# Optimization experiments

Hardware: AMD Instinct MI355X
Metric: run time of the kernel (lower is better)

## Reference

```python
import jax, jax.numpy as jnp
import numpy as np

E = 1024
H = 16
D = E // H
RANK = 4
NLANG = 8
SCALING = D ** -0.5


def _lowrank(r, s):
    # r: [rank, out], s: [rank, in] -> sum of outer products [out, in]
    return jnp.einsum('ro,ri->oi', r, s)


def setup_inputs() -> dict:
    key = jax.random.key(0)
    ks = jax.random.split(key, 20)
    std = np.sqrt(2.0 / (E + E)).astype(np.float32)
    std_lr = np.sqrt(0.02).astype(np.float32)
    inp = {
        'query': jax.random.normal(ks[0], (1024, 8, E), jnp.float32),
        'key': jax.random.normal(ks[1], (1024, 8, E), jnp.float32),
        'in_proj_weight_q': jax.random.normal(ks[2], (E, E), jnp.float32) * std,
        'in_proj_weight_kv': jax.random.normal(ks[3], (2 * E, E), jnp.float32) * std,
        'out_proj_weight': jax.random.normal(ks[4], (E, E), jnp.float32) * std,
        'r_q': jax.random.normal(ks[5], (NLANG, RANK, E), jnp.float32) * std_lr,
        's_q': jax.random.normal(ks[6], (NLANG, RANK, E), jnp.float32) * std_lr,
        'r_kv': jax.random.normal(ks[7], (NLANG, RANK, 2 * E), jnp.float32) * std_lr,
        's_kv': jax.random.normal(ks[8], (NLANG, RANK, E), jnp.float32) * std_lr,
        'r_o': jax.random.normal(ks[9], (NLANG, RANK, E), jnp.float32) * std_lr,
        's_o': jax.random.normal(ks[10], (NLANG, RANK, E), jnp.float32) * std_lr,
        # multiplicative factors: random +/-1 as in bernoulli init
        'rm_q': jnp.sign(jax.random.normal(ks[11], (NLANG, RANK, E), jnp.float32)),
        'sm_q': jnp.sign(jax.random.normal(ks[12], (NLANG, RANK, E), jnp.float32)),
        'rm_kv': jnp.sign(jax.random.normal(ks[13], (NLANG, RANK, 2 * E), jnp.float32)),
        'sm_kv': jnp.sign(jax.random.normal(ks[14], (NLANG, RANK, E), jnp.float32)),
        'rm_o': jnp.sign(jax.random.normal(ks[15], (NLANG, RANK, E), jnp.float32)),
        'sm_o': jnp.sign(jax.random.normal(ks[16], (NLANG, RANK, E), jnp.float32)),
        'src_indices': jax.random.randint(ks[17], (1,), 0, NLANG, jnp.int64 if jax.config.jax_enable_x64 else jnp.int32),
        'tgt_indices': jax.random.randint(ks[18], (1,), 0, NLANG, jnp.int64 if jax.config.jax_enable_x64 else jnp.int32),
    }
    return inp


def reference(query, key, in_proj_weight_q, in_proj_weight_kv, out_proj_weight,
              r_q, s_q, r_kv, s_kv, r_o, s_o,
              rm_q, sm_q, rm_kv, sm_kv, rm_o, sm_o,
              src_indices, tgt_indices):
    it = tgt_indices[0]
    isrc = src_indices[0]

    # multiplicative low-rank modulation then additive low-rank update
    Wq = in_proj_weight_q * _lowrank(rm_q[it], sm_q[isrc]) + _lowrank(r_q[it], s_q[isrc])
    Wkv = in_proj_weight_kv * _lowrank(rm_kv[it], sm_kv[isrc]) + _lowrank(r_kv[it], s_kv[isrc])
    Wo = out_proj_weight * _lowrank(rm_o[it], sm_o[isrc]) + _lowrank(r_o[it], s_o[isrc])

    lq, b, _ = query.shape
    lk = key.shape[0]

    # projections: F.linear(x, W) = x @ W.T
    q = jnp.einsum('lbe,fe->lbf', query, Wq) * SCALING          # [lq, b, E]
    kv = jnp.einsum('lbe,fe->lbf', key, Wkv)                    # [lk, b, 2E]
    k, v = kv[..., :E], kv[..., E:]

    # split heads: [len, b, E] -> [b*H, len, D]
    def to_heads(x, L):
        return x.reshape(L, b, H, D).transpose(1, 2, 0, 3).reshape(b * H, L, D)

    qh = to_heads(q, lq)
    kh = to_heads(k, lk)
    vh = to_heads(v, lk)

    scores = jnp.einsum('nqd,nkd->nqk', qh, kh)                 # [b*H, lq, lk]
    probs = jax.nn.softmax(scores, axis=-1)
    ctx = jnp.einsum('nqk,nkd->nqd', probs, vh)                 # [b*H, lq, D]

    # merge heads back to [lq, b, E]
    ctx = ctx.reshape(b, H, lq, D).transpose(2, 0, 1, 3).reshape(lq, b, E)
    out = jnp.einsum('lbe,fe->lbf', ctx, Wo)
    return out, probs
```

## Files before the change

### kernel.cpp

```cpp
#include <hip/hip_runtime.h>
#include <hip/hip_bf16.h>


typedef float  fx4 __attribute__((ext_vector_type(4)));
typedef short  sx8 __attribute__((ext_vector_type(8)));
typedef _Float16 hx8 __attribute__((ext_vector_type(8)));

__device__ __forceinline__ unsigned short f2h(float f) {
  return __builtin_bit_cast(unsigned short, (_Float16)f);
}
__device__ __forceinline__ float h2f(unsigned short h) {
  return (float)__builtin_bit_cast(_Float16, h);
}
__device__ __forceinline__ unsigned pk2h(float a, float b) {
  return __builtin_bit_cast(unsigned, __builtin_amdgcn_cvt_pkrtz(a, b));
}

__device__ __forceinline__ void gload_lds16(const void* g, void* l) {
  __builtin_amdgcn_global_load_lds((const __attribute__((address_space(1))) void*)g,
                                   (__attribute__((address_space(3))) void*)l, 16, 0, 0);
}

__device__ __forceinline__ fx4 mfma_h(sx8 a, sx8 b, fx4 c) {
  return __builtin_amdgcn_mfma_f32_16x16x32_f16(__builtin_bit_cast(hx8, a),
                                                __builtin_bit_cast(hx8, b), c, 0, 0, 0);
}

__device__ __forceinline__ void wait_vm_bar() {
  __builtin_amdgcn_sched_barrier(0);
  asm volatile("s_waitcnt vmcnt(0)" ::: "memory");
  __builtin_amdgcn_s_barrier();
  __builtin_amdgcn_sched_barrier(0);
}
__device__ __forceinline__ void wait_vm4_bar() {
  __builtin_amdgcn_sched_barrier(0);
  asm volatile("s_waitcnt vmcnt(4)" ::: "memory");
  __builtin_amdgcn_s_barrier();
  __builtin_amdgcn_sched_barrier(0);
}
__device__ __forceinline__ void bar_only() {
  __builtin_amdgcn_sched_barrier(0);
  __builtin_amdgcn_s_barrier();
  __builtin_amdgcn_sched_barrier(0);
}
__device__ __forceinline__ void bar_lgkm() {
  __builtin_amdgcn_sched_barrier(0);
  asm volatile("s_waitcnt lgkmcnt(0)" ::: "memory");
  __builtin_amdgcn_s_barrier();
  __builtin_amdgcn_sched_barrier(0);
}

__global__ void k_prep(
    const float* wq, const float* wkv, const float* wo,
    const float* r_q, const float* s_q, const float* r_kv, const float* s_kv,
    const float* r_o, const float* s_o,
    const float* rm_q, const float* sm_q, const float* rm_kv, const float* sm_kv,
    const float* rm_o, const float* sm_o,
    const int* src_i, const int* tgt_i,
    unsigned short* Wq16, unsigned short* Wkv16, unsigned short* Wo16,
    const float* query, const float* key,
    unsigned short* qh, unsigned short* kh)
{
  const int gid = blockIdx.x * 256 + threadIdx.x;
  if (gid >= 4194304) {
    const int cid = gid - 4194304;
    const bool isq = cid < 1048576;
    const size_t off = (size_t)(isq ? cid : cid - 1048576) * 8;
    const float* s = (isq ? query : key) + off;
    unsigned short* d = (isq ? qh : kh) + off;
    fx4 a = *(const fx4*)s, bv = *(const fx4*)(s + 4);
    sx8 h;
    #pragma unroll
    for (int j = 0; j < 4; ++j) { h[j] = (short)f2h(a[j]); h[4 + j] = (short)f2h(bv[j]); }
    *(sx8*)d = h;
    return;
  }
  const int it = tgt_i[0], is = src_i[0];
  const int mat = gid >> 20;
  const int idx = gid & 1048575;
  const int o = idx >> 10, i = idx & 1023;
  float lrm = 0.f, lr = 0.f;
  if (mat == 0) {
    #pragma unroll
    for (int r = 0; r < 4; ++r) {
      lrm += rm_q[(it * 4 + r) * 1024 + o] * sm_q[(is * 4 + r) * 1024 + i];
      lr  += r_q [(it * 4 + r) * 1024 + o] * s_q [(is * 4 + r) * 1024 + i];
    }
    Wq16[idx] = f2h((wq[idx] * lrm + lr) * 0.125f);
  } else if (mat == 1) {
    #pragma unroll
    for (int r = 0; r < 4; ++r) {
      lrm += rm_kv[(it * 4 + r) * 2048 + o] * sm_kv[(is * 4 + r) * 1024 + i];
      lr  += r_kv [(it * 4 + r) * 2048 + o] * s_kv [(is * 4 + r) * 1024 + i];
    }
    Wkv16[idx] = f2h(wkv[idx] * lrm + lr);
  } else if (mat == 2) {
    #pragma unroll
    for (int r = 0; r < 4; ++r) {
      lrm += rm_kv[(it * 4 + r) * 2048 + 1024 + o] * sm_kv[(is * 4 + r) * 1024 + i];
      lr  += r_kv [(it * 4 + r) * 2048 + 1024 + o] * s_kv [(is * 4 + r) * 1024 + i];
    }
    Wkv16[1048576 + idx] = f2h(wkv[1048576 + idx] * lrm + lr);
  } else {
    #pragma unroll
    for (int r = 0; r < 4; ++r) {
      lrm += rm_o[(it * 4 + r) * 1024 + o] * sm_o[(is * 4 + r) * 1024 + i];
      lr  += r_o [(it * 4 + r) * 1024 + o] * s_o [(is * 4 + r) * 1024 + i];
    }
    Wo16[idx] = f2h(wo[idx] * lrm + lr);
  }
}

__global__ __launch_bounds__(256, 2) void k_gemm_kvq(
    const unsigned short* qh, const unsigned short* kh,
    const unsigned short* Wq16, const unsigned short* Wkv16,
    unsigned short* k16, unsigned short* v16, unsigned short* q16)
{
  __shared__ unsigned short lds[2][2][4096];
  const int tid = threadIdx.x;
  const int l = tid & 63, wid = tid >> 6;
  const int wr = wid >> 1, wc = wid & 1;
  const int bid = blockIdx.x;
  const int logical = (bid & 7) * 192 + (bid >> 3);
  const int by = logical / 24, bx = logical % 24;
  const bool isKV = bx < 16;
  const unsigned short* A = isKV ? kh : qh;
  const unsigned short* B = isKV ? Wkv16 : Wq16;
  const int mBase = by * 128;
  const int nBase = (isKV ? bx : (bx - 16)) * 128;
  const int brow = tid >> 2, bc8 = (tid & 3) * 8;

  fx4 acc[4][4] = {};

  auto stage = [&](int buf, int kt) {
    const int kB = kt * 32;
    gload_lds16(B + (size_t)(nBase + brow) * 1024 + kB + bc8,      &lds[buf][1][tid * 8]);
    gload_lds16(B + (size_t)(nBase + 64 + brow) * 1024 + kB + bc8, &lds[buf][1][2048 + tid * 8]);
    gload_lds16(A + (size_t)(mBase + brow) * 1024 + kB + bc8,      &lds[buf][0][tid * 8]);
    gload_lds16(A + (size_t)(mBase + 64 + brow) * 1024 + kB + bc8, &lds[buf][0][2048 + tid * 8]);
  };

  auto compute = [&](int buf) {
    sx8 af[4], bfv[4];
    #pragma unroll
    for (int x = 0; x < 4; ++x) {
      af[x]  = *(const sx8*)&lds[buf][0][(wr * 64 + x * 16 + (l & 15)) * 32 + (l >> 4) * 8];
      bfv[x] = *(const sx8*)&lds[buf][1][(wc * 64 + x * 16 + (l & 15)) * 32 + (l >> 4) * 8];
    }
    #pragma unroll
    for (int mi = 0; mi < 4; ++mi)
      #pragma unroll
      for (int ni = 0; ni < 4; ++ni)
        acc[mi][ni] = mfma_h(af[mi], bfv[ni], acc[mi][ni]);
  };

  stage(0, 0);
  for (int kt = 0; kt < 32; ++kt) {
    const int buf = kt & 1;
    if (kt + 1 < 32) {
      stage(buf ^ 1, kt + 1);
      wait_vm4_bar();
    } else {
      wait_vm_bar();
    }
    compute(buf);
    bar_only();
  }

  #pragma unroll
  for (int mi = 0; mi < 4; ++mi)
    #pragma unroll
    for (int ni = 0; ni < 4; ++ni)
      #pragma unroll
      for (int i = 0; i < 4; ++i) {
        const size_t row = (size_t)(mBase + wr * 64 + mi * 16 + (l >> 4) * 4 + i);
        const int col = nBase + wc * 64 + ni * 16 + (l & 15);
        const unsigned short hv = f2h(acc[mi][ni][i]);
        if (isKV) {
          if (col < 1024) k16[row * 1024 + col] = hv;
          else            v16[row * 1024 + (col - 1024)] = hv;
        } else {
          q16[row * 1024 + col] = hv;
        }
      }
}

__global__ __launch_bounds__(256, 2) void k_gemm_out(
    const unsigned short* A, const unsigned short* B, float* Cf)
{
  __shared__ unsigned short lds[2][2][4096];
  const int tid = threadIdx.x;
  const int l = tid & 63, wid = tid >> 6;
  const int wr = wid >> 1, wc = wid & 1;
  const int bid = blockIdx.x;
  const int logical = (bid & 7) * 64 + (bid >> 3);
  const int mBase = (logical >> 3) * 128, nBase = (logical & 7) * 128;
  const int brow = tid >> 2, bc8 = (tid & 3) * 8;

  fx4 acc[4][4] = {};

  auto stage = [&](int buf, int kt) {
    const int kB = kt * 32;
    gload_lds16(B + (size_t)(nBase + brow) * 1024 + kB + bc8,      &lds[buf][1][tid * 8]);
    gload_lds16(B + (size_t)(nBase + 64 + brow) * 1024 + kB + bc8, &lds[buf][1][2048 + tid * 8]);
    gload_lds16(A + (size_t)(mBase + brow) * 1024 + kB + bc8,      &lds[buf][0][tid * 8]);
    gload_lds16(A + (size_t)(mBase + 64 + brow) * 1024 + kB + bc8, &lds[buf][0][2048 + tid * 8]);
  };

  auto compute = [&](int buf) {
    sx8 af[4], bfv[4];
    #pragma unroll
    for (int x = 0; x < 4; ++x) {
      af[x]  = *(const sx8*)&lds[buf][0][(wr * 64 + x * 16 + (l & 15)) * 32 + (l >> 4) * 8];
      bfv[x] = *(const sx8*)&lds[buf][1][(wc * 64 + x * 16 + (l & 15)) * 32 + (l >> 4) * 8];
    }
    #pragma unroll
    for (int mi = 0; mi < 4; ++mi)
      #pragma unroll
      for (int ni = 0; ni < 4; ++ni)
        acc[mi][ni] = mfma_h(af[mi], bfv[ni], acc[mi][ni]);
  };

  stage(0, 0);
  for (int kt = 0; kt < 32; ++kt) {
    const int buf = kt & 1;
    if (kt + 1 < 32) {
      stage(buf ^ 1, kt + 1);
      wait_vm4_bar();
    } else {
      wait_vm_bar();
    }
    compute(buf);
    bar_only();
  }

  #pragma unroll
  for (int mi = 0; mi < 4; ++mi)
    #pragma unroll
    for (int ni = 0; ni < 4; ++ni)
      #pragma unroll
      for (int i = 0; i < 4; ++i) {
        const size_t row = (size_t)(mBase + wr * 64 + mi * 16 + (l >> 4) * 4 + i);
        const int col = nBase + wc * 64 + ni * 16 + (l & 15);
        __builtin_nontemporal_store(acc[mi][ni][i], &Cf[row * 1024 + col]);
      }
}

__global__ __launch_bounds__(256) void k_vt(const unsigned short* v16, unsigned short* vT)
{
  __shared__ unsigned short t[64 * 72];
  const int tid = threadIdx.x;
  const int head = blockIdx.x >> 4, kb = blockIdx.x & 15;
  const int b = head >> 4, hh = head & 15;
  const int kl = tid >> 2, part = tid & 3;
  #pragma unroll
  for (int u = 0; u < 2; ++u) {
    sx8 v = *(const sx8*)&v16[(size_t)((kb * 64 + kl) * 8 + b) * 1024 + hh * 64 + part * 16 + u * 8];
    *(sx8*)&t[kl * 72 + part * 16 + u * 8] = v;
  }
  __syncthreads();
  const int dr = tid >> 2;
  unsigned short out[16];
  #pragma unroll
  for (int j = 0; j < 16; ++j) out[j] = t[(part * 16 + j) * 72 + dr];
  unsigned short* dst = vT + (size_t)((b * 16 + hh) * 64 + dr) * 1024 + kb * 64 + part * 16;
  *(sx8*)dst       = *(sx8*)&out[0];
  *(sx8*)(dst + 8) = *(sx8*)&out[8];
}

__global__ __launch_bounds__(512, 4) void k_attn(
    const unsigned short* q16, const unsigned short* k16, const unsigned short* vT,
    float* probsF, unsigned short* ctx)
{
  __shared__ __align__(16) unsigned short Pl[32768];
  __shared__ float redm[128], reds[128];

  const int tid = threadIdx.x, l = tid & 63, wid = tid >> 6;
  const int qg = wid >> 2, q4 = wid & 3;
  const int r = l & 15, g = l >> 4;
  const int bid = blockIdx.x;
  const int logical = (bid & 7) * 512 + (bid >> 3);
  const int head = logical >> 5, qb = logical & 31;
  const int b = head >> 4, hh = head & 15;

  auto stage_k = [&](int c) {
    #pragma unroll
    for (int rr = 0; rr < 8; ++rr) {
      const int e = rr * 512 + tid;
      const int lk = e >> 3, ch = e & 7;
      gload_lds16(k16 + (size_t)((c * 512 + lk) * 8 + b) * 1024 + hh * 64 + ((ch ^ (lk & 7)) * 8),
                  &Pl[e * 8]);
    }
  };

  sx8 qf0, qf1;
  {
    const int qrow = qb * 32 + qg * 16 + r;
    const size_t qoff = (size_t)(qrow * 8 + b) * 1024 + hh * 64 + g * 8;
    qf0 = *(const sx8*)&q16[qoff];
    qf1 = *(const sx8*)&q16[qoff + 32];
  }

  fx4 acc[16];
  #pragma unroll
  for (int s = 0; s < 16; ++s) acc[s] = fx4{0.f, 0.f, 0.f, 0.f};

  stage_k(0);
  wait_vm_bar();
  #pragma unroll
  for (int t = 0; t < 8; ++t) {
    const int lk = q4 * 128 + t * 16 + r;
    sx8 kb0 = *(const sx8*)&Pl[lk * 64 + ((g ^ (l & 7))) * 8];
    sx8 kb1 = *(const sx8*)&Pl[lk * 64 + (((4 + g) ^ (l & 7))) * 8];
    acc[t] = mfma_h(kb0, qf0, acc[t]);
    acc[t] = mfma_h(kb1, qf1, acc[t]);
  }
  bar_lgkm();
  stage_k(1);
  wait_vm_bar();
  #pragma unroll
  for (int t = 0; t < 8; ++t) {
    const int lk = q4 * 128 + t * 16 + r;
    sx8 kb0 = *(const sx8*)&Pl[lk * 64 + ((g ^ (l & 7))) * 8];
    sx8 kb1 = *(const sx8*)&Pl[lk * 64 + (((4 + g) ^ (l & 7))) * 8];
    acc[8 + t] = mfma_h(kb0, qf0, acc[8 + t]);
    acc[8 + t] = mfma_h(kb1, qf1, acc[8 + t]);
  }

  const int q = qg * 16 + r;
  float m = -3e38f;
  #pragma unroll
  for (int s = 0; s < 16; ++s)
    #pragma unroll
    for (int i = 0; i < 4; ++i) m = fmaxf(m, acc[s][i]);
  m = fmaxf(m, __shfl_xor(m, 16));
  m = fmaxf(m, __shfl_xor(m, 32));
  if (g == 0) redm[q * 4 + q4] = m;
  bar_lgkm();
  const float mf = fmaxf(fmaxf(redm[q * 4], redm[q * 4 + 1]),
                         fmaxf(redm[q * 4 + 2], redm[q * 4 + 3]));
  float ssum = 0.f;
  #pragma unroll
  for (int s = 0; s < 16; ++s)
    #pragma unroll
    for (int i = 0; i < 4; ++i) {
      const float e = __expf(acc[s][i] - mf);
      acc[s][i] = e;
      ssum += e;
    }
  ssum += __shfl_xor(ssum, 16);
  ssum += __shfl_xor(ssum, 32);
  if (g == 0) reds[q * 4 + q4] = ssum;
  bar_lgkm();
  const float inv = 1.0f / (reds[q * 4] + reds[q * 4 + 1] +
                            reds[q * 4 + 2] + reds[q * 4 + 3]);

  #pragma unroll
  for (int idx = 0; idx < 16; ++idx) {
    const int c = idx >> 3, t = idx & 7;
    const int k0 = c * 512 + q4 * 128 + t * 16 + g * 4;
    uint2 w;
    w.x = pk2h(acc[idx][0] * inv, acc[idx][1] * inv);
    w.y = pk2h(acc[idx][2] * inv, acc[idx][3] * inv);
    *(uint2*)&Pl[q * 1024 + (((k0 >> 3) ^ (q & 7)) << 3) + (k0 & 7)] = w;
  }
  bar_lgkm();

  if (wid < 4) {
    fx4 cacc0 = {}, cacc1 = {};
    const unsigned short* vrow = vT + (size_t)((b * 16 + hh) * 64 + wid * 16 + r) * 1024;
    #pragma unroll
    for (int cc = 0; cc < 32; ++cc) {
      const int k0 = cc * 32 + g * 8;
      sx8 vb  = *(const sx8*)&vrow[k0];
      sx8 pa0 = *(const sx8*)&Pl[(0 * 16 + r) * 1024 + (((k0 >> 3) ^ (r & 7)) << 3)];
      sx8 pa1 = *(const sx8*)&Pl[(16 + r) * 1024 + (((k0 >> 3) ^ ((16 + r) & 7)) << 3)];
      cacc0 = mfma_h(pa0, vb, cacc0);
      cacc1 = mfma_h(pa1, vb, cacc1);
    }
    const int d = wid * 16 + r;
    #pragma unroll
    for (int i = 0; i < 4; ++i) {
      const int q0 = qb * 32 + g * 4 + i;
      const int q1 = qb * 32 + 16 + g * 4 + i;
      ctx[(size_t)(q0 * 8 + b) * 1024 + hh * 64 + d] = f2h(cacc0[i]);
      ctx[(size_t)(q1 * 8 + b) * 1024 + hh * 64 + d] = f2h(cacc1[i]);
    }
  } else {
    const size_t pbase = (size_t)head * 1048576;
    const int rbase = (wid - 4) * 8;
    #pragma unroll
    for (int i = 0; i < 32; ++i) {
      const int row = rbase + (i >> 2);
      const int col = (i & 3) * 256 + l * 4;
      const int c16 = ((col >> 3) ^ (row & 7));
      const unsigned* raw = (const unsigned*)&Pl[row * 1024 + c16 * 8 + (col & 7)];
      const unsigned r0 = raw[0], r1 = raw[1];
      fx4 o;
      o[0] = h2f((unsigned short)(r0 & 0xffffu)); o[1] = h2f((unsigned short)(r0 >> 16));
      o[2] = h2f((unsigned short)(r1 & 0xffffu)); o[3] = h2f((unsigned short)(r1 >> 16));
      __builtin_nontemporal_store(o, (fx4*)&probsF[pbase + (size_t)(qb * 32 + row) * 1024 + col]);
    }
  }
}

extern "C" void kernel_launch(void* const* d_in, const int* in_sizes, int n_in,
                              void* d_out, int out_size, void* d_ws, size_t ws_size,
                              hipStream_t stream)
{
  const float* query = (const float*)d_in[0];
  const float* key   = (const float*)d_in[1];
  const float* wq    = (const float*)d_in[2];
  const float* wkv   = (const float*)d_in[3];
  const float* wo    = (const float*)d_in[4];
  const float* r_q   = (const float*)d_in[5];
  const float* s_q   = (const float*)d_in[6];
  const float* r_kv  = (const float*)d_in[7];
  const float* s_kv  = (const float*)d_in[8];
  const float* r_o   = (const float*)d_in[9];
  const float* s_o   = (const float*)d_in[10];
  const float* rm_q  = (const float*)d_in[11];
  const float* sm_q  = (const float*)d_in[12];
  const float* rm_kv = (const float*)d_in[13];
  const float* sm_kv = (const float*)d_in[14];
  const float* rm_o  = (const float*)d_in[15];
  const float* sm_o  = (const float*)d_in[16];
  const int* src_i   = (const int*)d_in[17];
  const int* tgt_i   = (const int*)d_in[18];

  unsigned short* ws16 = (unsigned short*)d_ws;
  const size_t M1 = 1048576, M8 = 8388608;
  unsigned short* Wq16  = ws16;
  unsigned short* Wkv16 = ws16 + M1;
  unsigned short* Wo16  = ws16 + 3 * M1;
  unsigned short* qh    = ws16 + 4 * M1;
  unsigned short* kh    = ws16 + 12 * M1;
  unsigned short* k16   = ws16 + 20 * M1;
  unsigned short* v16   = ws16 + 28 * M1;
  unsigned short* vT  = kh;
  unsigned short* ctx = qh;

  float* outF   = (float*)d_out;
  float* probsF = outF + M8;
  unsigned short* q16 = (unsigned short*)outF;

  k_prep<<<dim3(24576), dim3(256), 0, stream>>>(
      wq, wkv, wo, r_q, s_q, r_kv, s_kv, r_o, s_o,
      rm_q, sm_q, rm_kv, sm_kv, rm_o, sm_o, src_i, tgt_i,
      Wq16, Wkv16, Wo16, query, key, qh, kh);

  k_gemm_kvq<<<dim3(1536), dim3(256), 0, stream>>>(
      qh, kh, Wq16, Wkv16, k16, v16, q16);

  k_vt<<<dim3(2048), dim3(256), 0, stream>>>(v16, vT);

  k_attn<<<dim3(4096), dim3(512), 0, stream>>>(q16, k16, vT, probsF, ctx);

  k_gemm_out<<<dim3(512), dim3(256), 0, stream>>>(ctx, Wo16, outF);
}
```

Before: 272.7 us.

## Triple-buffer GEMM LDS pipeline and use nontemporal loads for streamed inputs

Both projection GEMMs move from double to triple buffering of LDS tiles, prefetching two k-steps ahead with a vmcnt(8) wait, and the launch bound rises to 3 blocks per CU. The aim is to hide more global-load latency behind MFMA work. Streaming reads in the prep and V-transpose kernels become nontemporal loads so they pollute the cache less. The extra buffer raises LDS use to 48KB per block and may constrain registers under the higher occupancy target.

```diff
diff --git a/kernel.cpp b/kernel.cpp
--- a/kernel.cpp
+++ b/kernel.cpp
@@ -29,6 +29,12 @@
 __device__ __forceinline__ void wait_vm_bar() {
   __builtin_amdgcn_sched_barrier(0);
   asm volatile("s_waitcnt vmcnt(0)" ::: "memory");
+  __builtin_amdgcn_s_barrier();
+  __builtin_amdgcn_sched_barrier(0);
+}
+__device__ __forceinline__ void wait_vm8_bar() {
+  __builtin_amdgcn_sched_barrier(0);
+  asm volatile("s_waitcnt vmcnt(8)" ::: "memory");
   __builtin_amdgcn_s_barrier();
   __builtin_amdgcn_sched_barrier(0);
 }
@@ -68,7 +74,8 @@
     const size_t off = (size_t)(isq ? cid : cid - 1048576) * 8;
     const float* s = (isq ? query : key) + off;
     unsigned short* d = (isq ? qh : kh) + off;
-    fx4 a = *(const fx4*)s, bv = *(const fx4*)(s + 4);
+    fx4 a = __builtin_nontemporal_load((const fx4*)s);
+    fx4 bv = __builtin_nontemporal_load((const fx4*)(s + 4));
     sx8 h;
     #pragma unroll
     for (int j = 0; j < 4; ++j) { h[j] = (short)f2h(a[j]); h[4 + j] = (short)f2h(bv[j]); }
@@ -86,37 +93,37 @@
       lrm += rm_q[(it * 4 + r) * 1024 + o] * sm_q[(is * 4 + r) * 1024 + i];
       lr  += r_q [(it * 4 + r) * 1024 + o] * s_q [(is * 4 + r) * 1024 + i];
     }
-    Wq16[idx] = f2h((wq[idx] * lrm + lr) * 0.125f);
+    Wq16[idx] = f2h((__builtin_nontemporal_load(&wq[idx]) * lrm + lr) * 0.125f);
   } else if (mat == 1) {
     #pragma unroll
     for (int r = 0; r < 4; ++r) {
       lrm += rm_kv[(it * 4 + r) * 2048 + o] * sm_kv[(is * 4 + r) * 1024 + i];
       lr  += r_kv [(it * 4 + r) * 2048 + o] * s_kv [(is * 4 + r) * 1024 + i];
     }
-    Wkv16[idx] = f2h(wkv[idx] * lrm + lr);
+    Wkv16[idx] = f2h(__builtin_nontemporal_load(&wkv[idx]) * lrm + lr);
   } else if (mat == 2) {
     #pragma unroll
     for (int r = 0; r < 4; ++r) {
       lrm += rm_kv[(it * 4 + r) * 2048 + 1024 + o] * sm_kv[(is * 4 + r) * 1024 + i];
       lr  += r_kv [(it * 4 + r) * 2048 + 1024 + o] * s_kv [(is * 4 + r) * 1024 + i];
     }
-    Wkv16[1048576 + idx] = f2h(wkv[1048576 + idx] * lrm + lr);
+    Wkv16[1048576 + idx] = f2h(__builtin_nontemporal_load(&wkv[1048576 + idx]) * lrm + lr);
   } else {
     #pragma unroll
     for (int r = 0; r < 4; ++r) {
       lrm += rm_o[(it * 4 + r) * 1024 + o] * sm_o[(is * 4 + r) * 1024 + i];
       lr  += r_o [(it * 4 + r) * 1024 + o] * s_o [(is * 4 + r) * 1024 + i];
     }
-    Wo16[idx] = f2h(wo[idx] * lrm + lr);
-  }
-}
-
-__global__ __launch_bounds__(256, 2) void k_gemm_kvq(
+    Wo16[idx] = f2h(__builtin_nontemporal_load(&wo[idx]) * lrm + lr);
+  }
+}
+
+__global__ __launch_bounds__(256, 3) void k_gemm_kvq(
     const unsigned short* qh, const unsigned short* kh,
     const unsigned short* Wq16, const unsigned short* Wkv16,
     unsigned short* k16, unsigned short* v16, unsigned short* q16)
 {
-  __shared__ unsigned short lds[2][2][4096];
+  __shared__ unsigned short lds[3][2][4096];
   const int tid = threadIdx.x;
   const int l = tid & 63, wid = tid >> 6;
   const int wr = wid >> 1, wc = wid & 1;
@@ -155,10 +162,13 @@
   };
 
   stage(0, 0);
+  stage(1, 1);
   for (int kt = 0; kt < 32; ++kt) {
-    const int buf = kt & 1;
-    if (kt + 1 < 32) {
-      stage(buf ^ 1, kt + 1);
+    const int buf = kt % 3;
+    if (kt + 2 < 32) {
+      stage((kt + 2) % 3, kt + 2);
+      wait_vm8_bar();
+    } else if (kt == 30) {
       wait_vm4_bar();
     } else {
       wait_vm_bar();
@@ -185,10 +195,10 @@
       }
 }
 
-__global__ __launch_bounds__(256, 2) void k_gemm_out(
+__global__ __launch_bounds__(256, 3) void k_gemm_out(
     const unsigned short* A, const unsigned short* B, float* Cf)
 {
-  __shared__ unsigned short lds[2][2][4096];
+  __shared__ unsigned short lds[3][2][4096];
   const int tid = threadIdx.x;
   const int l = tid & 63, wid = tid >> 6;
   const int wr = wid >> 1, wc = wid & 1;
@@ -222,10 +232,13 @@
   };
 
   stage(0, 0);
+  stage(1, 1);
   for (int kt = 0; kt < 32; ++kt) {
-    const int buf = kt & 1;
-    if (kt + 1 < 32) {
-      stage(buf ^ 1, kt + 1);
+    const int buf = kt % 3;
+    if (kt + 2 < 32) {
+      stage((kt + 2) % 3, kt + 2);
+      wait_vm8_bar();
+    } else if (kt == 30) {
       wait_vm4_bar();
     } else {
       wait_vm_bar();
@@ -255,7 +268,8 @@
   const int kl = tid >> 2, part = tid & 3;
   #pragma unroll
   for (int u = 0; u < 2; ++u) {
-    sx8 v = *(const sx8*)&v16[(size_t)((kb * 64 + kl) * 8 + b) * 1024 + hh * 64 + part * 16 + u * 8];
+    sx8 v = __builtin_nontemporal_load(
+        (const sx8*)&v16[(size_t)((kb * 64 + kl) * 8 + b) * 1024 + hh * 64 + part * 16 + u * 8]);
     *(sx8*)&t[kl * 72 + part * 16 + u * 8] = v;
   }
   __syncthreads();
```

New measurement: 279.4 us. 2.5% more time.

## Fuse V transpose into KV projection GEMM epilogue and use nontemporal loads in prep

Applied to the files above, without the earlier changes.

The V half of the KV projection GEMM now writes its tile transposed through shared memory straight into the per-head vT layout, so the separate k_vt kernel is gone. This drops one launch and a full write-plus-read round trip of the V tensor through global memory. The prep kernel also switches its streaming fp32 loads to nontemporal loads. In exchange, the GEMM needs extra LDS for the transpose buffer, which may lower occupancy, and its V-tile epilogue issues 16 strided 2-byte LDS reads per output chunk.

```diff
diff --git a/kernel.cpp b/kernel.cpp
--- a/kernel.cpp
+++ b/kernel.cpp
@@ -68,7 +68,8 @@
     const size_t off = (size_t)(isq ? cid : cid - 1048576) * 8;
     const float* s = (isq ? query : key) + off;
     unsigned short* d = (isq ? qh : kh) + off;
-    fx4 a = *(const fx4*)s, bv = *(const fx4*)(s + 4);
+    fx4 a = __builtin_nontemporal_load((const fx4*)s);
+    fx4 bv = __builtin_nontemporal_load((const fx4*)(s + 4));
     sx8 h;
     #pragma unroll
     for (int j = 0; j < 4; ++j) { h[j] = (short)f2h(a[j]); h[4 + j] = (short)f2h(bv[j]); }
@@ -86,37 +87,38 @@
       lrm += rm_q[(it * 4 + r) * 1024 + o] * sm_q[(is * 4 + r) * 1024 + i];
       lr  += r_q [(it * 4 + r) * 1024 + o] * s_q [(is * 4 + r) * 1024 + i];
     }
-    Wq16[idx] = f2h((wq[idx] * lrm + lr) * 0.125f);
+    Wq16[idx] = f2h((__builtin_nontemporal_load(&wq[idx]) * lrm + lr) * 0.125f);
   } else if (mat == 1) {
     #pragma unroll
     for (int r = 0; r < 4; ++r) {
       lrm += rm_kv[(it * 4 + r) * 2048 + o] * sm_kv[(is * 4 + r) * 1024 + i];
       lr  += r_kv [(it * 4 + r) * 2048 + o] * s_kv [(is * 4 + r) * 1024 + i];
     }
-    Wkv16[idx] = f2h(wkv[idx] * lrm + lr);
+    Wkv16[idx] = f2h(__builtin_nontemporal_load(&wkv[idx]) * lrm + lr);
   } else if (mat == 2) {
     #pragma unroll
     for (int r = 0; r < 4; ++r) {
       lrm += rm_kv[(it * 4 + r) * 2048 + 1024 + o] * sm_kv[(is * 4 + r) * 1024 + i];
       lr  += r_kv [(it * 4 + r) * 2048 + 1024 + o] * s_kv [(is * 4 + r) * 1024 + i];
     }
-    Wkv16[1048576 + idx] = f2h(wkv[1048576 + idx] * lrm + lr);
+    Wkv16[1048576 + idx] = f2h(__builtin_nontemporal_load(&wkv[1048576 + idx]) * lrm + lr);
   } else {
     #pragma unroll
     for (int r = 0; r < 4; ++r) {
       lrm += rm_o[(it * 4 + r) * 1024 + o] * sm_o[(is * 4 + r) * 1024 + i];
       lr  += r_o [(it * 4 + r) * 1024 + o] * s_o [(is * 4 + r) * 1024 + i];
     }
-    Wo16[idx] = f2h(wo[idx] * lrm + lr);
+    Wo16[idx] = f2h(__builtin_nontemporal_load(&wo[idx]) * lrm + lr);
   }
 }
 
 __global__ __launch_bounds__(256, 2) void k_gemm_kvq(
     const unsigned short* qh, const unsigned short* kh,
     const unsigned short* Wq16, const unsigned short* Wkv16,
-    unsigned short* k16, unsigned short* v16, unsigned short* q16)
+    unsigned short* k16, unsigned short* vT, unsigned short* q16)
 {
   __shared__ unsigned short lds[2][2][4096];
+  __shared__ unsigned short Tt[128 * 136];
   const int tid = threadIdx.x;
   const int l = tid & 63, wid = tid >> 6;
   const int wr = wid >> 1, wc = wid & 1;
@@ -167,22 +169,46 @@
     bar_only();
   }
 
-  #pragma unroll
-  for (int mi = 0; mi < 4; ++mi)
-    #pragma unroll
-    for (int ni = 0; ni < 4; ++ni)
-      #pragma unroll
-      for (int i = 0; i < 4; ++i) {
-        const size_t row = (size_t)(mBase + wr * 64 + mi * 16 + (l >> 4) * 4 + i);
-        const int col = nBase + wc * 64 + ni * 16 + (l & 15);
-        const unsigned short hv = f2h(acc[mi][ni][i]);
-        if (isKV) {
-          if (col < 1024) k16[row * 1024 + col] = hv;
-          else            v16[row * 1024 + (col - 1024)] = hv;
-        } else {
-          q16[row * 1024 + col] = hv;
+  if (isKV && nBase >= 1024) {
+    #pragma unroll
+    for (int mi = 0; mi < 4; ++mi)
+      #pragma unroll
+      for (int ni = 0; ni < 4; ++ni)
+        #pragma unroll
+        for (int i = 0; i < 4; ++i) {
+          const int cl = wc * 64 + ni * 16 + (l & 15);
+          const int rl = wr * 64 + mi * 16 + (l >> 4) * 4 + i;
+          Tt[cl * 136 + rl] = f2h(acc[mi][ni][i]);
         }
-      }
+    bar_lgkm();
+    const int h0 = (nBase - 1024) >> 6;
+    const int lkb = mBase >> 3;
+    #pragma unroll
+    for (int j4 = 0; j4 < 4; ++j4) {
+      const int jj = j4 * 256 + tid;
+      const int vcol = jj >> 3, b = jj & 7;
+      const int h = h0 + (vcol >> 6), d = vcol & 63;
+      unsigned short out[16];
+      #pragma unroll
+      for (int t = 0; t < 16; ++t) out[t] = Tt[vcol * 136 + t * 8 + b];
+      unsigned short* dst = vT + (size_t)((b * 16 + h) * 64 + d) * 1024 + lkb;
+      *(sx8*)dst       = *(sx8*)&out[0];
+      *(sx8*)(dst + 8) = *(sx8*)&out[8];
+    }
+  } else {
+    #pragma unroll
+    for (int mi = 0; mi < 4; ++mi)
+      #pragma unroll
+      for (int ni = 0; ni < 4; ++ni)
+        #pragma unroll
+        for (int i = 0; i < 4; ++i) {
+          const size_t row = (size_t)(mBase + wr * 64 + mi * 16 + (l >> 4) * 4 + i);
+          const int col = nBase + wc * 64 + ni * 16 + (l & 15);
+          const unsigned short hv = f2h(acc[mi][ni][i]);
+          if (isKV) k16[row * 1024 + col] = hv;
+          else      q16[row * 1024 + col] = hv;
+        }
+  }
 }
 
 __global__ __launch_bounds__(256, 2) void k_gemm_out(
@@ -244,28 +270,6 @@
         const int col = nBase + wc * 64 + ni * 16 + (l & 15);
         __builtin_nontemporal_store(acc[mi][ni][i], &Cf[row * 1024 + col]);
       }
-}
-
-__global__ __launch_bounds__(256) void k_vt(const unsigned short* v16, unsigned short* vT)
-{
-  __shared__ unsigned short t[64 * 72];
-  const int tid = threadIdx.x;
-  const int head = blockIdx.x >> 4, kb = blockIdx.x & 15;
-  const int b = head >> 4, hh = head & 15;
-  const int kl = tid >> 2, part = tid & 3;
-  #pragma unroll
-  for (int u = 0; u < 2; ++u) {
-    sx8 v = *(const sx8*)&v16[(size_t)((kb * 64 + kl) * 8 + b) * 1024 + hh * 64 + part * 16 + u * 8];
-    *(sx8*)&t[kl * 72 + part * 16 + u * 8] = v;
-  }
-  __syncthreads();
-  const int dr = tid >> 2;
-  unsigned short out[16];
-  #pragma unroll
-  for (int j = 0; j < 16; ++j) out[j] = t[(part * 16 + j) * 72 + dr];
-  unsigned short* dst = vT + (size_t)((b * 16 + hh) * 64 + dr) * 1024 + kb * 64 + part * 16;
-  *(sx8*)dst       = *(sx8*)&out[0];
-  *(sx8*)(dst + 8) = *(sx8*)&out[8];
 }
 
 __global__ __launch_bounds__(512, 4) void k_attn(
@@ -436,8 +440,7 @@
   unsigned short* qh    = ws16 + 4 * M1;
   unsigned short* kh    = ws16 + 12 * M1;
   unsigned short* k16   = ws16 + 20 * M1;
-  unsigned short* v16   = ws16 + 28 * M1;
-  unsigned short* vT  = kh;
+  unsigned short* vT    = ws16 + 28 * M1;
   unsigned short* ctx = qh;
 
   float* outF   = (float*)d_out;
@@ -450,9 +453,7 @@
       Wq16, Wkv16, Wo16, query, key, qh, kh);
 
   k_gemm_kvq<<<dim3(1536), dim3(256), 0, stream>>>(
-      qh, kh, Wq16, Wkv16, k16, v16, q16);
-
-  k_vt<<<dim3(2048), dim3(256), 0, stream>>>(v16, vT);
+      qh, kh, Wq16, Wkv16, k16, vT, q16);
 
   k_attn<<<dim3(4096), dim3(512), 0, stream>>>(q16, k16, vT, probsF, ctx);
 
```

Measured after the change: 287.5 us. 5.4% more time.
